# Kernel optimization log

Measured on AMD Instinct MI355X. Metric: run time of the kernel, lower is better.

The kernel has to match this reference:

```python
import jax, jax.numpy as jnp
import numpy as np

N_NODES = 50000
N_EDGES = 1600000
IN_CH = 32
HID = 64
EPS = 1e-12


def setup_inputs() -> dict:
    key = jax.random.key(0)
    ks = jax.random.split(key, 10)
    x = jax.random.normal(ks[0], (N_NODES, IN_CH), dtype=jnp.float32)
    edge_index = jax.random.randint(ks[1], (2, N_EDGES), 0, N_NODES, dtype=jnp.int64)

    def lin(k, fan_in, fan_out):
        bound = 1.0 / np.sqrt(fan_in)
        return jax.random.uniform(k, (fan_in, fan_out), jnp.float32, -bound, bound)

    params = {
        # SAGEConv layer 0: lin_l (aggregated neighbors, with bias), lin_r (root, no bias)
        'Wl0': lin(ks[2], IN_CH, HID), 'b0': jnp.zeros((HID,), jnp.float32),
        'Wr0': lin(ks[3], IN_CH, HID),
        # SAGEConv layer 1
        'Wl1': lin(ks[4], HID, HID), 'b1': jnp.zeros((HID,), jnp.float32),
        'Wr1': lin(ks[5], HID, HID),
        # classifier: Linear(64,32) -> ReLU -> Linear(32,1)
        'Wc1': lin(ks[6], HID, HID // 2), 'bc1': jnp.zeros((HID // 2,), jnp.float32),
        'Wc2': lin(ks[7], HID // 2, 1), 'bc2': jnp.zeros((1,), jnp.float32),
    }
    return {'x': x, 'edge_index': edge_index, **params}


def _sage_conv(x, src, dst, Wl, Wr, b):
    # gather messages from source nodes, mean-aggregate at destination
    msg = x[src]                                            # [E, C]
    agg = jax.ops.segment_sum(msg, dst, num_segments=N_NODES)
    cnt = jax.ops.segment_sum(jnp.ones((src.shape[0], 1), x.dtype), dst,
                              num_segments=N_NODES)
    mean = agg / jnp.maximum(cnt, 1.0)                      # [N, C]
    out = mean @ Wl + x @ Wr + b                            # [N, H]
    # normalize=True -> L2 row-normalization (F.normalize, eps=1e-12)
    nrm = jnp.linalg.norm(out, axis=-1, keepdims=True)
    return out / jnp.maximum(nrm, EPS)


def reference(x, edge_index, Wl0, b0, Wr0, Wl1, b1, Wr1, Wc1, bc1, Wc2, bc2):
    src, dst = edge_index[0], edge_index[1]
    h = _sage_conv(x, src, dst, Wl0, Wr0, b0)
    h = jax.nn.relu(h)                                      # dropout inactive (eval)
    h = _sage_conv(h, src, dst, Wl1, Wr1, b1)
    h = jax.nn.relu(h @ Wc1 + bc1)
    logits = (h @ Wc2 + bc2).squeeze(-1)                    # [N]
    return logits
```

## Files before the change

kernel.cpp:

```cpp
#include <hip/hip_runtime.h>

static constexpr int N_NODES = 50000;
static constexpr int N_EDGES = 1600000;
static constexpr int CIN = 32;
static constexpr int HID = 64;
static constexpr int NTB = N_NODES / 16;
static constexpr int NBUCK = (N_NODES + 31) / 32;
static constexpr int NB_BLD = 128;
static constexpr int EPB2 = N_EDGES / NB_BLD;

__device__ __forceinline__ unsigned short f2bf(float f) {
    unsigned int u = __float_as_uint(f);
    u = (u + 0x7fffu + ((u >> 16) & 1u)) >> 16;
    return (unsigned short)u;
}
__device__ __forceinline__ float bfhi(unsigned int u) { return __uint_as_float(u & 0xffff0000u); }
__device__ __forceinline__ float bflo(unsigned int u) { return __uint_as_float(u << 16); }


__global__ void __launch_bounds__(256)
histB_kernel(const int* __restrict__ ei, int* __restrict__ part) {
    __shared__ int hist[NBUCK];
    for (int i = threadIdx.x; i < NBUCK; i += 256) hist[i] = 0;
    __syncthreads();
    const int base = blockIdx.x * EPB2;
    const int t = threadIdx.x;
    for (int i0 = 0; i0 < EPB2; i0 += 1024) {
        int d[4];
#pragma unroll
        for (int k = 0; k < 4; ++k) {
            const int i = i0 + k * 256 + t;
            d[k] = (i < EPB2) ? ei[N_EDGES + base + i] : -1;
        }
#pragma unroll
        for (int k = 0; k < 4; ++k)
            if (d[k] >= 0) atomicAdd(&hist[d[k] >> 5], 1);
    }
    __syncthreads();
    for (int i = threadIdx.x; i < NBUCK; i += 256)
        part[i * NB_BLD + blockIdx.x] = hist[i];
}

__global__ void __launch_bounds__(NB_BLD)
scanA_kernel(int* __restrict__ part, int* __restrict__ btot) {
    __shared__ int s[NB_BLD];
    const int t = threadIdx.x;
    const int v = part[blockIdx.x * NB_BLD + t];
    s[t] = v;
    __syncthreads();
    for (int st = 1; st < NB_BLD; st <<= 1) {
        int u = (t >= st) ? s[t - st] : 0;
        __syncthreads();
        s[t] += u;
        __syncthreads();
    }
    part[blockIdx.x * NB_BLD + t] = s[t] - v;
    if (t == NB_BLD - 1) btot[blockIdx.x] = s[NB_BLD - 1];
}

__global__ void __launch_bounds__(1024)
scanB_kernel(const int* __restrict__ btot, int* __restrict__ bstart) {
    __shared__ int pairs[1024];
    __shared__ int v0s[1024];
    const int t = threadIdx.x;
    const int i0 = 2 * t, i1 = 2 * t + 1;
    const int v0 = (i0 < NBUCK) ? btot[i0] : 0;
    const int v1 = (i1 < NBUCK) ? btot[i1] : 0;
    v0s[t] = v0;
    const int p = v0 + v1;
    pairs[t] = p;
    __syncthreads();
    for (int st = 1; st < 1024; st <<= 1) {
        int u = (t >= st) ? pairs[t - st] : 0;
        __syncthreads();
        pairs[t] += u;
        __syncthreads();
    }
    const int base = pairs[t] - p;
    if (i0 < NBUCK) bstart[i0] = base;
    if (i1 < NBUCK) bstart[i1] = base + v0s[t];
    if (t == 1023) bstart[NBUCK] = pairs[1023];
}

__global__ void __launch_bounds__(256)
scatterB_kernel(const int* __restrict__ ei, const int* __restrict__ part,
                const int* __restrict__ bstart, unsigned* __restrict__ bentry) {
    __shared__ int cur[NBUCK];
    for (int i = threadIdx.x; i < NBUCK; i += 256)
        cur[i] = bstart[i] + part[i * NB_BLD + blockIdx.x];
    __syncthreads();
    const int base = blockIdx.x * EPB2;
    const int t = threadIdx.x;
    for (int i0 = 0; i0 < EPB2; i0 += 1024) {
        int s[4], d[4];
#pragma unroll
        for (int k = 0; k < 4; ++k) {
            const int i = i0 + k * 256 + t;
            const bool val = i < EPB2;
            s[k] = val ? ei[base + i] : 0;
            d[k] = val ? ei[N_EDGES + base + i] : -1;
        }
#pragma unroll
        for (int k = 0; k < 4; ++k)
            if (d[k] >= 0) {
                const int pos = atomicAdd(&cur[d[k] >> 5], 1);
                bentry[pos] = ((unsigned)s[k] << 5) | (unsigned)(d[k] & 31);
            }
    }
}

__global__ void __launch_bounds__(256)
sortW_kernel(const unsigned* __restrict__ bentry, const int* __restrict__ bstart,
             int* __restrict__ sorted_src, int* __restrict__ off) {
    __shared__ int cnt[32];
    __shared__ int base[33];
    __shared__ int cur[32];
    const int b = blockIdx.x, t = threadIdx.x;
    const int s0 = bstart[b], s1 = bstart[b + 1];
    if (t < 32) cnt[t] = 0;
    __syncthreads();
    for (int i = s0 + t; i < s1; i += 256)
        atomicAdd(&cnt[bentry[i] & 31], 1);
    __syncthreads();
    if (t == 0) {
        int run = s0;
#pragma unroll
        for (int l = 0; l < 32; ++l) { base[l] = run; cur[l] = run; run += cnt[l]; }
        base[32] = run;
    }
    __syncthreads();
    if (t <= 32) {
        const int gn = b * 32 + t;
        if (gn <= N_NODES) off[gn] = base[t];
    }
    for (int i = s0 + t; i < s1; i += 256) {
        const unsigned e = bentry[i];
        const int pos = atomicAdd(&cur[e & 31], 1);
        sorted_src[pos] = (int)(e >> 5);
    }
}

__global__ void __launch_bounds__(256)
agg0_kernel(const float* __restrict__ x,
            const int* __restrict__ off, const int* __restrict__ src,
            unsigned short* __restrict__ mean0b) {
    const int node = blockIdx.x * 4 + (threadIdx.x >> 6);
    const int lane = threadIdx.x & 63;
    if (node >= N_NODES) return;
    const int e0 = off[node], e1 = off[node + 1];
    const int deg = e1 - e0;
    const int grp = lane >> 3, cg = lane & 7;

    float a[4] = {0, 0, 0, 0};
    for (int base = e0; base < e1; base += 64) {
        const int cnt = min(64, e1 - base);
        const int p = base + lane;
        const int sidx = (p < e1) ? src[p] : 0;
        const int nb = (cnt + 7) >> 3;
        float4 u[8];
#pragma unroll
        for (int t = 0; t < 8; ++t) u[t] = make_float4(0.f, 0.f, 0.f, 0.f);
#pragma unroll
        for (int t = 0; t < 8; ++t) {
            if (t < nb) {
                const int pos = (t << 3) | grp;
                const int s = __shfl(sidx, pos);
                if (pos < cnt)
                    u[t] = *reinterpret_cast<const float4*>(x + (size_t)s * CIN + cg * 4);
            }
        }
#pragma unroll
        for (int t = 0; t < 8; ++t) {
            a[0] += u[t].x; a[1] += u[t].y; a[2] += u[t].z; a[3] += u[t].w;
        }
    }
#pragma unroll
    for (int j = 0; j < 4; ++j) {
        a[j] += __shfl_xor(a[j], 8);
        a[j] += __shfl_xor(a[j], 16);
        a[j] += __shfl_xor(a[j], 32);
    }
    const float inv = 1.0f / fmaxf((float)deg, 1.0f);
    if (grp == 0) {
        uint2 o;
        o.x = (unsigned)f2bf(a[0] * inv) | ((unsigned)f2bf(a[1] * inv) << 16);
        o.y = (unsigned)f2bf(a[2] * inv) | ((unsigned)f2bf(a[3] * inv) << 16);
        reinterpret_cast<uint2*>(mean0b)[node * 8 + cg] = o;
    }
}

__global__ void __launch_bounds__(256)
agg1_kernel(const unsigned short* __restrict__ hb,
            const int* __restrict__ off, const int* __restrict__ src,
            float* __restrict__ mean1f) {
    const int node = blockIdx.x * 4 + (threadIdx.x >> 6);
    const int lane = threadIdx.x & 63;
    if (node >= N_NODES) return;
    const int e0 = off[node], e1 = off[node + 1];
    const int deg = e1 - e0;
    const int grp = lane >> 3, cg = lane & 7;

    float a[8] = {0, 0, 0, 0, 0, 0, 0, 0};
    for (int base = e0; base < e1; base += 64) {
        const int cnt = min(64, e1 - base);
        const int p = base + lane;
        const int sidx = (p < e1) ? src[p] : 0;
        const int nb = (cnt + 7) >> 3;
        uint4 u[8];
#pragma unroll
        for (int t = 0; t < 8; ++t) u[t] = make_uint4(0u, 0u, 0u, 0u);
#pragma unroll
        for (int t = 0; t < 8; ++t) {
            if (t < nb) {
                const int pos = (t << 3) | grp;
                const int s = __shfl(sidx, pos);
                if (pos < cnt)
                    u[t] = *reinterpret_cast<const uint4*>(hb + (size_t)s * HID + cg * 8);
            }
        }
#pragma unroll
        for (int t = 0; t < 8; ++t) {
            a[0] += bflo(u[t].x); a[1] += bfhi(u[t].x);
            a[2] += bflo(u[t].y); a[3] += bfhi(u[t].y);
            a[4] += bflo(u[t].z); a[5] += bfhi(u[t].z);
            a[6] += bflo(u[t].w); a[7] += bfhi(u[t].w);
        }
    }
#pragma unroll
    for (int j = 0; j < 8; ++j) {
        a[j] += __shfl_xor(a[j], 8);
        a[j] += __shfl_xor(a[j], 16);
        a[j] += __shfl_xor(a[j], 32);
    }
    const float inv = 1.0f / fmaxf((float)deg, 1.0f);
    if (grp == 0) {
        float4 o1 = make_float4(a[0] * inv, a[1] * inv, a[2] * inv, a[3] * inv);
        float4 o2 = make_float4(a[4] * inv, a[5] * inv, a[6] * inv, a[7] * inv);
        float4* dst = reinterpret_cast<float4*>(mean1f + (size_t)node * HID + cg * 8);
        dst[0] = o1; dst[1] = o2;
    }
}

__global__ void __launch_bounds__(256)
transform0_kernel(const float* __restrict__ x,
                  const unsigned short* __restrict__ mean0b,
                  const float* __restrict__ Wl0, const float* __restrict__ Wr0,
                  const float* __restrict__ b0,
                  unsigned short* __restrict__ hb) {
    __shared__ float sWl[CIN * HID];
    __shared__ float sWr[CIN * HID];
    __shared__ float sMin[16 * CIN];
    __shared__ float sXin[16 * CIN];
    const int t = threadIdx.x;
    const int blk = blockIdx.x;
    reinterpret_cast<float4*>(sWl)[t]       = reinterpret_cast<const float4*>(Wl0)[t];
    reinterpret_cast<float4*>(sWl)[t + 256] = reinterpret_cast<const float4*>(Wl0)[t + 256];
    reinterpret_cast<float4*>(sWr)[t]       = reinterpret_cast<const float4*>(Wr0)[t];
    reinterpret_cast<float4*>(sWr)[t + 256] = reinterpret_cast<const float4*>(Wr0)[t + 256];
    {
        const unsigned u = reinterpret_cast<const unsigned*>(mean0b)[blk * 256 + t];
        sMin[2 * t]     = bflo(u);
        sMin[2 * t + 1] = bfhi(u);
    }
    if (t < 128)
        reinterpret_cast<float4*>(sXin)[t] =
            reinterpret_cast<const float4*>(x + (size_t)blk * 16 * CIN)[t];
    __syncthreads();

    const int n = t >> 4, cg = t & 15;
    const float4 bv = reinterpret_cast<const float4*>(b0)[cg];
    float a[4] = {bv.x, bv.y, bv.z, bv.w};
#pragma unroll
    for (int k = 0; k < CIN; ++k) {
        const float m  = sMin[n * CIN + k];
        const float xx = sXin[n * CIN + k];
        const float4 wl = reinterpret_cast<const float4*>(sWl + k * HID)[cg];
        const float4 wr = reinterpret_cast<const float4*>(sWr + k * HID)[cg];
        a[0] = fmaf(m, wl.x, fmaf(xx, wr.x, a[0]));
        a[1] = fmaf(m, wl.y, fmaf(xx, wr.y, a[1]));
        a[2] = fmaf(m, wl.z, fmaf(xx, wr.z, a[2]));
        a[3] = fmaf(m, wl.w, fmaf(xx, wr.w, a[3]));
    }
    float ss = a[0] * a[0] + a[1] * a[1] + a[2] * a[2] + a[3] * a[3];
    ss += __shfl_xor(ss, 1);
    ss += __shfl_xor(ss, 2);
    ss += __shfl_xor(ss, 4);
    ss += __shfl_xor(ss, 8);
    const float sc = 1.0f / fmaxf(sqrtf(ss), 1e-12f);
    uint2 o;
    o.x = (unsigned)f2bf(fmaxf(a[0] * sc, 0.f)) | ((unsigned)f2bf(fmaxf(a[1] * sc, 0.f)) << 16);
    o.y = (unsigned)f2bf(fmaxf(a[2] * sc, 0.f)) | ((unsigned)f2bf(fmaxf(a[3] * sc, 0.f)) << 16);
    reinterpret_cast<uint2*>(hb)[(size_t)(blk * 16 + n) * 16 + cg] = o;
}

__global__ void __launch_bounds__(256)
transform1_kernel(const unsigned short* __restrict__ hb,
                  const float* __restrict__ mean1f,
                  const float* __restrict__ Wl1, const float* __restrict__ Wr1,
                  const float* __restrict__ b1,
                  const float* __restrict__ Wc1, const float* __restrict__ bc1,
                  const float* __restrict__ Wc2, const float* __restrict__ bc2,
                  float* __restrict__ out) {
    __shared__ float sWl[HID * HID];
    __shared__ float sWr[HID * HID];
    __shared__ float sWc[HID * 32];
    __shared__ float sMin[16 * HID];
    __shared__ float sHin[16 * HID];
    __shared__ float sV[16 * HID];
    const int t = threadIdx.x;
    const int blk = blockIdx.x;
#pragma unroll
    for (int i = 0; i < 4; ++i) {
        reinterpret_cast<float4*>(sWl)[t + 256 * i] = reinterpret_cast<const float4*>(Wl1)[t + 256 * i];
        reinterpret_cast<float4*>(sWr)[t + 256 * i] = reinterpret_cast<const float4*>(Wr1)[t + 256 * i];
    }
#pragma unroll
    for (int i = 0; i < 2; ++i)
        reinterpret_cast<float4*>(sWc)[t + 256 * i] = reinterpret_cast<const float4*>(Wc1)[t + 256 * i];
    reinterpret_cast<float4*>(sMin)[t] =
        reinterpret_cast<const float4*>(mean1f + (size_t)blk * 16 * HID)[t];
    {
        const uint2 hu = reinterpret_cast<const uint2*>(hb)[(size_t)blk * 256 + t];
        sHin[4 * t]     = bflo(hu.x);
        sHin[4 * t + 1] = bfhi(hu.x);
        sHin[4 * t + 2] = bflo(hu.y);
        sHin[4 * t + 3] = bfhi(hu.y);
    }
    __syncthreads();

    const int n = t >> 4, cg = t & 15;
    const float4 bv = reinterpret_cast<const float4*>(b1)[cg];
    float a[4] = {bv.x, bv.y, bv.z, bv.w};
#pragma unroll
    for (int k = 0; k < HID; ++k) {
        const float m  = sMin[n * HID + k];
        const float hh = sHin[n * HID + k];
        const float4 wl = reinterpret_cast<const float4*>(sWl + k * HID)[cg];
        const float4 wr = reinterpret_cast<const float4*>(sWr + k * HID)[cg];
        a[0] = fmaf(m, wl.x, fmaf(hh, wr.x, a[0]));
        a[1] = fmaf(m, wl.y, fmaf(hh, wr.y, a[1]));
        a[2] = fmaf(m, wl.z, fmaf(hh, wr.z, a[2]));
        a[3] = fmaf(m, wl.w, fmaf(hh, wr.w, a[3]));
    }
    float ss = a[0] * a[0] + a[1] * a[1] + a[2] * a[2] + a[3] * a[3];
    ss += __shfl_xor(ss, 1);
    ss += __shfl_xor(ss, 2);
    ss += __shfl_xor(ss, 4);
    ss += __shfl_xor(ss, 8);
    const float sc = 1.0f / fmaxf(sqrtf(ss), 1e-12f);
    sV[n * HID + 4 * cg + 0] = a[0] * sc;
    sV[n * HID + 4 * cg + 1] = a[1] * sc;
    sV[n * HID + 4 * cg + 2] = a[2] * sc;
    sV[n * HID + 4 * cg + 3] = a[3] * sc;
    __syncthreads();

    float c1a = bc1[cg], c1b = bc1[cg + 16];
#pragma unroll
    for (int k = 0; k < HID; ++k) {
        const float vv = sV[n * HID + k];
        c1a = fmaf(vv, sWc[k * 32 + cg], c1a);
        c1b = fmaf(vv, sWc[k * 32 + cg + 16], c1b);
    }
    float pp = fmaxf(c1a, 0.f) * Wc2[cg] + fmaxf(c1b, 0.f) * Wc2[cg + 16];
    pp += __shfl_xor(pp, 1);
    pp += __shfl_xor(pp, 2);
    pp += __shfl_xor(pp, 4);
    pp += __shfl_xor(pp, 8);
    if (cg == 0) out[blk * 16 + n] = pp + bc2[0];
}

extern "C" void kernel_launch(void* const* d_in, const int* in_sizes, int n_in,
                              void* d_out, int out_size, void* d_ws, size_t ws_size,
                              hipStream_t stream) {
    const float* x   = (const float*)d_in[0];
    const int*   ei  = (const int*)d_in[1];
    const float* Wl0 = (const float*)d_in[2];
    const float* b0  = (const float*)d_in[3];
    const float* Wr0 = (const float*)d_in[4];
    const float* Wl1 = (const float*)d_in[5];
    const float* b1  = (const float*)d_in[6];
    const float* Wr1 = (const float*)d_in[7];
    const float* Wc1 = (const float*)d_in[8];
    const float* bc1 = (const float*)d_in[9];
    const float* Wc2 = (const float*)d_in[10];
    const float* bc2 = (const float*)d_in[11];
    float* out = (float*)d_out;

    float* W = (float*)d_ws;
    int*            part   = (int*)W;
    int*            btot   = (int*)(W + 200064);
    int*            bstart = (int*)(W + 201632);
    unsigned*       bentry = (unsigned*)(W + 1600000);
    unsigned short* mean0b = (unsigned short*)W;
    float*          mean1f = W;
    int*            sorted_src = (int*)(W + 3200000);
    int*            off    = (int*)(W + 4800000);
    unsigned short* hb     = (unsigned short*)(W + 4850016);

    const int T = 256;
    histB_kernel<<<NB_BLD, T, 0, stream>>>(ei, part);
    scanA_kernel<<<NBUCK, NB_BLD, 0, stream>>>(part, btot);
    scanB_kernel<<<1, 1024, 0, stream>>>(btot, bstart);
    scatterB_kernel<<<NB_BLD, T, 0, stream>>>(ei, part, bstart, bentry);
    sortW_kernel<<<NBUCK, T, 0, stream>>>(bentry, bstart, sorted_src, off);

    const int ngrid = (N_NODES + 3) / 4;
    agg0_kernel<<<ngrid, T, 0, stream>>>(x, off, sorted_src, mean0b);
    transform0_kernel<<<NTB, T, 0, stream>>>(x, mean0b, Wl0, Wr0, b0, hb);
    agg1_kernel<<<ngrid, T, 0, stream>>>(hb, off, sorted_src, mean1f);
    transform1_kernel<<<NTB, T, 0, stream>>>(hb, mean1f, Wl1, Wr1, b1,
                                             Wc1, bc1, Wc2, bc2, out);
}
```

Baseline: 158.7 us.

## Gather bf16 features and split layer-1 table into cache-sized halves

Adds a kernel that casts x to bf16 so the layer-0 neighbor gather reads half the bytes. Layer-0 output is stored as two 32-channel bf16 tables, and layer-1 aggregation runs as two passes over them, so each gathered table (about 3.2 MB) is more likely to stay cache-resident. The cost is an extra cast kernel, a second full pass over the edge list and offsets, bf16 rounding of the input features, and an extra launch.

```diff
diff --git a/kernel.cpp b/kernel.cpp
--- a/kernel.cpp
+++ b/kernel.cpp
@@ -17,6 +17,18 @@
 __device__ __forceinline__ float bfhi(unsigned int u) { return __uint_as_float(u & 0xffff0000u); }
 __device__ __forceinline__ float bflo(unsigned int u) { return __uint_as_float(u << 16); }
 
+__global__ void __launch_bounds__(256)
+xcast_kernel(const float* __restrict__ x, unsigned short* __restrict__ xb) {
+    const int i = blockIdx.x * 256 + threadIdx.x;
+    if (i < N_NODES * CIN / 4) {
+        const float4 v = reinterpret_cast<const float4*>(x)[i];
+        uint2 o;
+        o.x = (unsigned)f2bf(v.x) | ((unsigned)f2bf(v.y) << 16);
+        o.y = (unsigned)f2bf(v.z) | ((unsigned)f2bf(v.w) << 16);
+        reinterpret_cast<uint2*>(xb)[i] = o;
+    }
+}
+
 
 __global__ void __launch_bounds__(256)
 histB_kernel(const int* __restrict__ ei, int* __restrict__ part) {
@@ -141,7 +153,7 @@
 }
 
 __global__ void __launch_bounds__(256)
-agg0_kernel(const float* __restrict__ x,
+agg0_kernel(const unsigned short* __restrict__ xb,
             const int* __restrict__ off, const int* __restrict__ src,
             unsigned short* __restrict__ mean0b) {
     const int node = blockIdx.x * 4 + (threadIdx.x >> 6);
@@ -157,21 +169,22 @@
         const int p = base + lane;
         const int sidx = (p < e1) ? src[p] : 0;
         const int nb = (cnt + 7) >> 3;
-        float4 u[8];
-#pragma unroll
-        for (int t = 0; t < 8; ++t) u[t] = make_float4(0.f, 0.f, 0.f, 0.f);
+        uint2 u[8];
+#pragma unroll
+        for (int t = 0; t < 8; ++t) u[t] = make_uint2(0u, 0u);
 #pragma unroll
         for (int t = 0; t < 8; ++t) {
             if (t < nb) {
                 const int pos = (t << 3) | grp;
                 const int s = __shfl(sidx, pos);
                 if (pos < cnt)
-                    u[t] = *reinterpret_cast<const float4*>(x + (size_t)s * CIN + cg * 4);
+                    u[t] = *reinterpret_cast<const uint2*>(xb + (size_t)s * 32 + cg * 4);
             }
         }
 #pragma unroll
         for (int t = 0; t < 8; ++t) {
-            a[0] += u[t].x; a[1] += u[t].y; a[2] += u[t].z; a[3] += u[t].w;
+            a[0] += bflo(u[t].x); a[1] += bfhi(u[t].x);
+            a[2] += bflo(u[t].y); a[3] += bfhi(u[t].y);
         }
     }
 #pragma unroll
@@ -190,9 +203,9 @@
 }
 
 __global__ void __launch_bounds__(256)
-agg1_kernel(const unsigned short* __restrict__ hb,
-            const int* __restrict__ off, const int* __restrict__ src,
-            float* __restrict__ mean1f) {
+agg1p_kernel(const unsigned short* __restrict__ tbl,
+             const int* __restrict__ off, const int* __restrict__ src,
+             float* __restrict__ dstbase) {
     const int node = blockIdx.x * 4 + (threadIdx.x >> 6);
     const int lane = threadIdx.x & 63;
     if (node >= N_NODES) return;
@@ -200,44 +213,40 @@
     const int deg = e1 - e0;
     const int grp = lane >> 3, cg = lane & 7;
 
-    float a[8] = {0, 0, 0, 0, 0, 0, 0, 0};
+    float a[4] = {0, 0, 0, 0};
     for (int base = e0; base < e1; base += 64) {
         const int cnt = min(64, e1 - base);
         const int p = base + lane;
         const int sidx = (p < e1) ? src[p] : 0;
         const int nb = (cnt + 7) >> 3;
-        uint4 u[8];
-#pragma unroll
-        for (int t = 0; t < 8; ++t) u[t] = make_uint4(0u, 0u, 0u, 0u);
+        uint2 u[8];
+#pragma unroll
+        for (int t = 0; t < 8; ++t) u[t] = make_uint2(0u, 0u);
 #pragma unroll
         for (int t = 0; t < 8; ++t) {
             if (t < nb) {
                 const int pos = (t << 3) | grp;
                 const int s = __shfl(sidx, pos);
                 if (pos < cnt)
-                    u[t] = *reinterpret_cast<const uint4*>(hb + (size_t)s * HID + cg * 8);
+                    u[t] = *reinterpret_cast<const uint2*>(tbl + (size_t)s * 32 + cg * 4);
             }
         }
 #pragma unroll
         for (int t = 0; t < 8; ++t) {
             a[0] += bflo(u[t].x); a[1] += bfhi(u[t].x);
             a[2] += bflo(u[t].y); a[3] += bfhi(u[t].y);
-            a[4] += bflo(u[t].z); a[5] += bfhi(u[t].z);
-            a[6] += bflo(u[t].w); a[7] += bfhi(u[t].w);
-        }
-    }
-#pragma unroll
-    for (int j = 0; j < 8; ++j) {
+        }
+    }
+#pragma unroll
+    for (int j = 0; j < 4; ++j) {
         a[j] += __shfl_xor(a[j], 8);
         a[j] += __shfl_xor(a[j], 16);
         a[j] += __shfl_xor(a[j], 32);
     }
     const float inv = 1.0f / fmaxf((float)deg, 1.0f);
     if (grp == 0) {
-        float4 o1 = make_float4(a[0] * inv, a[1] * inv, a[2] * inv, a[3] * inv);
-        float4 o2 = make_float4(a[4] * inv, a[5] * inv, a[6] * inv, a[7] * inv);
-        float4* dst = reinterpret_cast<float4*>(mean1f + (size_t)node * HID + cg * 8);
-        dst[0] = o1; dst[1] = o2;
+        float4 o = make_float4(a[0] * inv, a[1] * inv, a[2] * inv, a[3] * inv);
+        *reinterpret_cast<float4*>(dstbase + (size_t)node * HID + cg * 4) = o;
     }
 }
 
@@ -246,7 +255,8 @@
                   const unsigned short* __restrict__ mean0b,
                   const float* __restrict__ Wl0, const float* __restrict__ Wr0,
                   const float* __restrict__ b0,
-                  unsigned short* __restrict__ hb) {
+                  unsigned short* __restrict__ hbA,
+                  unsigned short* __restrict__ hbB) {
     __shared__ float sWl[CIN * HID];
     __shared__ float sWr[CIN * HID];
     __shared__ float sMin[16 * CIN];
@@ -290,11 +300,14 @@
     uint2 o;
     o.x = (unsigned)f2bf(fmaxf(a[0] * sc, 0.f)) | ((unsigned)f2bf(fmaxf(a[1] * sc, 0.f)) << 16);
     o.y = (unsigned)f2bf(fmaxf(a[2] * sc, 0.f)) | ((unsigned)f2bf(fmaxf(a[3] * sc, 0.f)) << 16);
-    reinterpret_cast<uint2*>(hb)[(size_t)(blk * 16 + n) * 16 + cg] = o;
-}
-
-__global__ void __launch_bounds__(256)
-transform1_kernel(const unsigned short* __restrict__ hb,
+    const int g = blk * 16 + n;
+    unsigned short* dst = (cg < 8) ? hbA : hbB;
+    reinterpret_cast<uint2*>(dst)[(size_t)g * 8 + (cg & 7)] = o;
+}
+
+__global__ void __launch_bounds__(256)
+transform1_kernel(const unsigned short* __restrict__ hbA,
+                  const unsigned short* __restrict__ hbB,
                   const float* __restrict__ mean1f,
                   const float* __restrict__ Wl1, const float* __restrict__ Wr1,
                   const float* __restrict__ b1,
@@ -320,7 +333,10 @@
     reinterpret_cast<float4*>(sMin)[t] =
         reinterpret_cast<const float4*>(mean1f + (size_t)blk * 16 * HID)[t];
     {
-        const uint2 hu = reinterpret_cast<const uint2*>(hb)[(size_t)blk * 256 + t];
+        const int g = blk * 16 + (t >> 4);
+        const int sub = t & 15;
+        const unsigned short* part = (sub < 8) ? hbA : hbB;
+        const uint2 hu = reinterpret_cast<const uint2*>(part)[(size_t)g * 8 + (sub & 7)];
         sHin[4 * t]     = bflo(hu.x);
         sHin[4 * t + 1] = bfhi(hu.x);
         sHin[4 * t + 2] = bflo(hu.y);
@@ -395,9 +411,12 @@
     float*          mean1f = W;
     int*            sorted_src = (int*)(W + 3200000);
     int*            off    = (int*)(W + 4800000);
-    unsigned short* hb     = (unsigned short*)(W + 4850016);
+    unsigned short* hbA    = (unsigned short*)(W + 4850016);
+    unsigned short* hbB    = (unsigned short*)(W + 5650016);
+    unsigned short* xb     = (unsigned short*)(W + 6450016);
 
     const int T = 256;
+    xcast_kernel<<<(N_NODES * CIN / 4 + T - 1) / T, T, 0, stream>>>(x, xb);
     histB_kernel<<<NB_BLD, T, 0, stream>>>(ei, part);
     scanA_kernel<<<NBUCK, NB_BLD, 0, stream>>>(part, btot);
     scanB_kernel<<<1, 1024, 0, stream>>>(btot, bstart);
@@ -405,9 +424,10 @@
     sortW_kernel<<<NBUCK, T, 0, stream>>>(bentry, bstart, sorted_src, off);
 
     const int ngrid = (N_NODES + 3) / 4;
-    agg0_kernel<<<ngrid, T, 0, stream>>>(x, off, sorted_src, mean0b);
-    transform0_kernel<<<NTB, T, 0, stream>>>(x, mean0b, Wl0, Wr0, b0, hb);
-    agg1_kernel<<<ngrid, T, 0, stream>>>(hb, off, sorted_src, mean1f);
-    transform1_kernel<<<NTB, T, 0, stream>>>(hb, mean1f, Wl1, Wr1, b1,
+    agg0_kernel<<<ngrid, T, 0, stream>>>(xb, off, sorted_src, mean0b);
+    transform0_kernel<<<NTB, T, 0, stream>>>(x, mean0b, Wl0, Wr0, b0, hbA, hbB);
+    agg1p_kernel<<<ngrid, T, 0, stream>>>(hbA, off, sorted_src, mean1f);
+    agg1p_kernel<<<ngrid, T, 0, stream>>>(hbB, off, sorted_src, mean1f + 32);
+    transform1_kernel<<<NTB, T, 0, stream>>>(hbA, hbB, mean1f, Wl1, Wr1, b1,
                                              Wc1, bc1, Wc2, bc2, out);
 }
```

After: 169.0 us. 6.5% more time.
